# Optimization experiments

Measured on AMD Instinct MI355X. Metric: run time of the kernel, lower is better.

Reference implementation:

```python
import jax, jax.numpy as jnp
import numpy as np

H = 4  # num_heads
EPS = 1e-12


def _mhsa(x, wq, bq, wk, bk, wv, bv, wo, bo):
    # x: [N, A, B, E]; attention over axis B within each (N, A)
    N, A, B, E = x.shape
    d = E // H
    q = (x @ wq + bq).reshape(N, A, B, H, d)
    k = (x @ wk + bk).reshape(N, A, B, H, d)
    v = (x @ wv + bv).reshape(N, A, B, H, d)
    s = jnp.einsum('naqhd,nakhd->nahqk', q, k) / (d ** 0.5)
    a = jax.nn.softmax(s, axis=-1)
    o = jnp.einsum('nahqk,nakhd->naqhd', a, v).reshape(N, A, B, E)
    return o @ wo + bo


def setup_inputs() -> dict:
    key = jax.random.key(0)
    ks = jax.random.split(key, 32)
    N, C, T, V, E, NC = 1024, 3, 30, 14, 64, 7
    g = lambda k, shape, s=0.05: (jax.random.normal(k, shape, dtype=jnp.float32) * s)
    inp = {
        'x_joint': jax.random.normal(ks[0], (N, C, T, V), dtype=jnp.float32),
        'x_vel': jax.random.normal(ks[1], (N, C, T, V), dtype=jnp.float32),
        'je_w': g(ks[2], (C, E)), 'je_b': g(ks[3], (E,)),
        've_w': g(ks[4], (C, E)), 've_b': g(ks[5], (E,)),
        'joint_emb': g(ks[6], (V, E)), 'frame_emb': g(ks[7], (T, E)),
        'proj_w': g(ks[8], (3 * E, E)), 'proj_b': g(ks[9], (E,)),
        'gcn_w1': g(ks[10], (E, E)), 'gcn_b1': g(ks[11], (E,)),
        'gcn_w2': g(ks[12], (E, E)), 'gcn_b2': g(ks[13], (E,)),
        'sa_wq': g(ks[14], (E, E)), 'sa_bq': g(ks[15], (E,)),
        'sa_wk': g(ks[16], (E, E)), 'sa_bk': g(ks[17], (E,)),
        'sa_wv': g(ks[18], (E, E)), 'sa_bv': g(ks[19], (E,)),
        'sa_wo': g(ks[20], (E, E)), 'sa_bo': g(ks[21], (E,)),
        'ta_wq': g(ks[22], (E, E)), 'ta_bq': g(ks[23], (E,)),
        'ta_wk': g(ks[24], (E, E)), 'ta_bk': g(ks[25], (E,)),
        'ta_wv': g(ks[26], (E, E)), 'ta_bv': g(ks[27], (E,)),
        'ta_wo': g(ks[28], (E, E)), 'ta_bo': g(ks[29], (E,)),
        'fc_w': g(ks[30], (E, NC)), 'fc_b': g(ks[31], (NC,)),
    }
    return inp


def reference(x_joint, x_vel, je_w, je_b, ve_w, ve_b, joint_emb, frame_emb,
              proj_w, proj_b, gcn_w1, gcn_b1, gcn_w2, gcn_b2,
              sa_wq, sa_bq, sa_wk, sa_bk, sa_wv, sa_bv, sa_wo, sa_bo,
              ta_wq, ta_bq, ta_wk, ta_bk, ta_wv, ta_bv, ta_wo, ta_bo,
              fc_w, fc_b):
    N, C, T, V = x_joint.shape
    E = je_w.shape[1]
    # 1x1 convs (pointwise over channels) -> [N, T, V, E]
    f = (jnp.einsum('nctv,ce->ntve', x_joint, je_w) + je_b
         + jnp.einsum('nctv,ce->ntve', x_vel, ve_w) + ve_b)
    jE = jnp.broadcast_to(joint_emb[None, None, :, :], (N, T, V, E))
    fE = jnp.broadcast_to(frame_emb[None, :, None, :], (N, T, V, E))
    feat = jnp.concatenate([f, jE, fE], axis=-1) @ proj_w + proj_b  # [N,T,V,E]
    # attention adjacency over joints per frame
    nf = feat / jnp.maximum(jnp.linalg.norm(feat, axis=-1, keepdims=True), EPS)
    adj = jax.nn.softmax(nf @ jnp.swapaxes(nf, -1, -2), axis=-1)  # [N,T,V,V]
    feat = adj @ feat
    feat = jax.nn.relu(feat @ gcn_w1 + gcn_b1) @ gcn_w2 + gcn_b2
    # spatial attention (over V) with residual
    feat = _mhsa(feat, sa_wq, sa_bq, sa_wk, sa_bk, sa_wv, sa_bv, sa_wo, sa_bo) + feat
    # temporal attention (over T) with residual
    ft = jnp.swapaxes(feat, 1, 2)  # [N,V,T,E]
    ft = _mhsa(ft, ta_wq, ta_bq, ta_wk, ta_bk, ta_wv, ta_bv, ta_wo, ta_bo) + ft
    feat = jnp.swapaxes(ft, 1, 2)  # [N,T,V,E]
    pooled = jnp.max(feat, axis=(1, 2))  # adaptive max pool over (T,V)
    return pooled @ fc_w + fc_b
```

## Files before the change

### kernel.cpp

```cpp
#include <hip/hip_runtime.h>
#include <math.h>

#define C_ 3
#define T_ 30
#define V_ 14
#define E_ 64
#define H_ 4
#define D_ 16
#define NC_ 7

#define SW_ 72
#define SV_ 20
#define ARN_ 6272

typedef unsigned short u16;
typedef __attribute__((ext_vector_type(8))) short bf16x8;
typedef __attribute__((ext_vector_type(4))) short bf16x4;
typedef __attribute__((ext_vector_type(4))) float f32x4;
typedef __attribute__((ext_vector_type(16))) float f32x16;

__device__ __forceinline__ float4 f4_load(const float* p) {
    return *reinterpret_cast<const float4*>(p);
}
__device__ __forceinline__ float4 f4_add(float4 a, float4 b) {
    return make_float4(a.x + b.x, a.y + b.y, a.z + b.z, a.w + b.w);
}
__device__ __forceinline__ float4 f4_fma(float a, float4 b, float4 c) {
    c.x = fmaf(a, b.x, c.x); c.y = fmaf(a, b.y, c.y);
    c.z = fmaf(a, b.z, c.z); c.w = fmaf(a, b.w, c.w); return c;
}
__device__ __forceinline__ u16 f2bf(float x) {
    union { __bf16 b; u16 u; } cv;
    cv.b = (__bf16)x;
    return cv.u;
}
__device__ __forceinline__ uint2 pack4bf(float4 f) {
    return make_uint2((unsigned)f2bf(f.x) | ((unsigned)f2bf(f.y) << 16),
                      (unsigned)f2bf(f.z) | ((unsigned)f2bf(f.w) << 16));
}
__device__ __forceinline__ f32x16 f16z() {
    return (f32x16){0.f,0.f,0.f,0.f, 0.f,0.f,0.f,0.f, 0.f,0.f,0.f,0.f, 0.f,0.f,0.f,0.f};
}
__device__ __forceinline__ bf16x8 ld_frag8(const u16* p) {
    bf16x4 lo = *(const bf16x4*)p;
    bf16x4 hi = *(const bf16x4*)(p + 4);
    return __builtin_shufflevector(lo, hi, 0, 1, 2, 3, 4, 5, 6, 7);
}

__global__ void k_setup(const float* __restrict__ je_w, const float* __restrict__ je_b,
                        const float* __restrict__ ve_w, const float* __restrict__ ve_b,
                        const float* __restrict__ joint_emb, const float* __restrict__ frame_emb,
                        const float* __restrict__ proj_w, const float* __restrict__ proj_b,
                        const float* __restrict__ twq, const float* __restrict__ twk,
                        const float* __restrict__ twv, const float* __restrict__ two,
                        const float* __restrict__ sw1, const float* __restrict__ sw2,
                        const float* __restrict__ swq, const float* __restrict__ swk,
                        const float* __restrict__ swv, const float* __restrict__ swo,
                        float* __restrict__ tab) {
    int e = threadIdx.x;
    int b = blockIdx.x;
    if (b >= 1 && b <= 10) {
        int m = b - 1;
        const float* Ws[10] = {twq, twk, twv, two, sw1, sw2, swq, swk, swv, swo};
        const float* W = Ws[m];
        u16* wt = (u16*)(tab + 3200);
        for (int i = 0; i < E_; ++i)
            wt[m * 4096 + e * 64 + i] = f2bf(W[i * E_ + e]);
        return;
    }
    if (b >= 11) {
        float bias = proj_b[e];
        for (int i = 0; i < E_; ++i) bias += (je_b[i] + ve_b[i]) * proj_w[i * E_ + e];
        int t0 = (b - 11) * 10;
        for (int t = t0; t < t0 + 10; ++t) {
            float s = bias;
            for (int i = 0; i < E_; ++i) s += frame_emb[t * E_ + i] * proj_w[(128 + i) * E_ + e];
            tab[1280 + t * E_ + e] = s;
        }
        return;
    }
    for (int c = 0; c < C_; ++c) {
        float aj = 0.f, av = 0.f;
        for (int i = 0; i < E_; ++i) {
            float p0 = proj_w[i * E_ + e];
            aj += je_w[c * E_ + i] * p0;
            av += ve_w[c * E_ + i] * p0;
        }
        tab[c * E_ + e] = aj;
        tab[192 + c * E_ + e] = av;
    }
    for (int v = 0; v < V_; ++v) {
        float s = 0.f;
        for (int i = 0; i < E_; ++i) s += joint_emb[v * E_ + i] * proj_w[(64 + i) * E_ + e];
        tab[384 + v * E_ + e] = s;
    }
}

__global__ __launch_bounds__(128) void k_spatial(
    const float* __restrict__ xj, const float* __restrict__ xv,
    const float* __restrict__ tab, const u16* __restrict__ wt16,
    const float* __restrict__ b1, const float* __restrict__ b2,
    const float* __restrict__ bq, const float* __restrict__ bk,
    const float* __restrict__ bv, const float* __restrict__ bo,
    float* __restrict__ feat1) {
    int ntb0 = blockIdx.x * 2;
    int tid = threadIdx.x;
    int wid = tid >> 6;
    int lane = tid & 63;
    int dcol = lane & 15;
    int kgrp = (lane >> 4) & 3;
    int trow4 = kgrp * 4;
    int e4 = dcol << 2;
    int r4 = kgrp;
    int l32 = lane & 31;
    int half = (lane >> 5) & 1;

    const u16* w1T = wt16 + 4 * 4096;
    const u16* w2T = wt16 + 5 * 4096;
    const u16* wqT = wt16 + 6 * 4096;
    const u16* wkT = wt16 + 7 * 4096;
    const u16* wvT = wt16 + 8 * 4096;
    const u16* woT = wt16 + 9 * 4096;

    __shared__ __align__(16) u16 sm[2 * ARN_];

    int tt[2];
    tt[0] = ntb0 % T_;
    tt[1] = (ntb0 + 1) % T_;
    int nn0 = ntb0 / T_, nn1 = (ntb0 + 1) / T_;

    for (int o = tid; o < 2 * 2 * C_ * V_; o += 128) {
        int tl = o / (2 * C_ * V_);
        int rem = o % (2 * C_ * V_);
        int s = rem / (C_ * V_);
        int r2 = rem % (C_ * V_);
        int c = r2 / V_, v = r2 % V_;
        const float* src = s ? xv : xj;
        int n = tl ? nn1 : nn0;
        float* xs = (float*)(sm + tl * ARN_ + 4992);
        xs[(s * C_ + c) * V_ + v] = src[((size_t)(n * C_ + c) * T_ + tt[tl]) * V_ + v];
    }
    __syncthreads();

    {
        float4 AJ[C_], AV[C_];
#pragma unroll
        for (int c = 0; c < C_; ++c) {
            AJ[c] = f4_load(tab + c * E_ + e4);
            AV[c] = f4_load(tab + 192 + c * E_ + e4);
        }
#pragma unroll
        for (int tl = 0; tl < 2; ++tl) {
            u16* A = sm + tl * ARN_;
            u16* feat16 = A;
            u16* fT16 = A + 1152;
            float* xs = (float*)(A + 4992);
            float4 F = f4_load(tab + 1280 + tt[tl] * E_ + e4);
#pragma unroll
            for (int j = 0; j < 2; ++j) {
                int q = r4 + 4 * (wid * 2 + j);
                if (q < V_) {
                    float4 s = f4_add(F, f4_load(tab + 384 + q * E_ + e4));
#pragma unroll
                    for (int c = 0; c < C_; ++c) {
                        s = f4_fma(xs[(0 * C_ + c) * V_ + q], AJ[c], s);
                        s = f4_fma(xs[(1 * C_ + c) * V_ + q], AV[c], s);
                    }
                    *(uint2*)&feat16[q * SW_ + e4] = pack4bf(s);
                    fT16[(e4 + 0) * SV_ + q] = f2bf(s.x);
                    fT16[(e4 + 1) * SV_ + q] = f2bf(s.y);
                    fT16[(e4 + 2) * SV_ + q] = f2bf(s.z);
                    fT16[(e4 + 3) * SV_ + q] = f2bf(s.w);
                }
            }
        }
        {
            u16* fT16 = sm + wid * ARN_ + 1152;
            fT16[lane * SV_ + 14] = 0;
            fT16[lane * SV_ + 15] = 0;
        }
    }
    __syncthreads();

    {
        u16* A = sm + wid * ARN_;
        u16* feat16 = A;
        float* adjraw = (float*)(A + 2432);
        bf16x8 f0 = *(bf16x8*)&feat16[dcol * SW_ + kgrp * 8];
        bf16x8 f1 = *(bf16x8*)&feat16[dcol * SW_ + 32 + kgrp * 8];
        f32x4 d = (f32x4){0.f, 0.f, 0.f, 0.f};
        d = __builtin_amdgcn_mfma_f32_16x16x32_bf16(f0, f0, d, 0, 0, 0);
        d = __builtin_amdgcn_mfma_f32_16x16x32_bf16(f1, f1, d, 0, 0, 0);
#pragma unroll
        for (int r = 0; r < 4; ++r) {
            int row = trow4 + r;
            if (row < V_) adjraw[row * 18 + dcol] = d[r];
        }
    }
    __syncthreads();

    if (lane < 4 * V_) {
        u16* A = sm + wid * ARN_;
        float* adjraw = (float*)(A + 2432);
        u16* adjs16 = A + 3712;
        int row = lane >> 2, g = lane & 3;
        float iq = 1.0f / fmaxf(sqrtf(adjraw[row * 18 + row]), 1e-12f);
        float c[4];
        float m = -1e30f;
#pragma unroll
        for (int j = 0; j < 4; ++j) {
            int k = g * 4 + j;
            if (k < V_) {
                float ik = 1.0f / fmaxf(sqrtf(adjraw[k * 18 + k]), 1e-12f);
                c[j] = adjraw[row * 18 + k] * iq * ik;
            } else {
                c[j] = -1e30f;
            }
            m = fmaxf(m, c[j]);
        }
        m = fmaxf(m, __shfl_xor(m, 1));
        m = fmaxf(m, __shfl_xor(m, 2));
        float su = 0.f;
#pragma unroll
        for (int j = 0; j < 4; ++j) { c[j] = __expf(c[j] - m); su += c[j]; }
        su += __shfl_xor(su, 1);
        su += __shfl_xor(su, 2);
        float iv = 1.f / su;
#pragma unroll
        for (int j = 0; j < 4; ++j) {
            int k = g * 4 + j;
            if (k < V_) adjs16[row * SV_ + k] = f2bf(c[j] * iv);
        }
        if (g == 3) {
            adjs16[row * SV_ + 14] = 0;
            adjs16[row * SV_ + 15] = 0;
        }
    }
    __syncthreads();

#pragma unroll
    for (int tl = 0; tl < 2; ++tl) {
        u16* A = sm + tl * ARN_;
        u16* adjs16 = A + 3712;
        u16* fT16 = A + 1152;
        u16* g1in = A + 2432;
        bf16x8 aA = ld_frag8(&adjs16[l32 * SV_ + half * 8]);
        int nt = wid;
        bf16x8 bB = ld_frag8(&fT16[(nt * 32 + l32) * SV_ + half * 8]);
        f32x16 g = f16z();
        g = __builtin_amdgcn_mfma_f32_32x32x16_bf16(aA, bB, g, 0, 0, 0);
#pragma unroll
        for (int reg = 0; reg < 16; ++reg) {
            int row = (reg & 3) + 8 * (reg >> 2) + 4 * half;
            if (row < V_) g1in[row * SW_ + nt * 32 + l32] = f2bf(g[reg]);
        }
    }
    __syncthreads();

#pragma unroll
    for (int tl = 0; tl < 2; ++tl) {
        u16* A = sm + tl * ARN_;
        u16* g1in = A + 2432;
        u16* g1out = A;
        bf16x8 a0 = *(bf16x8*)&g1in[dcol * SW_ + kgrp * 8];
        bf16x8 a1 = *(bf16x8*)&g1in[dcol * SW_ + 32 + kgrp * 8];
#pragma unroll
        for (int j = 0; j < 2; ++j) {
            int nt = wid * 2 + j;
            int col = nt * 16 + dcol;
            float bb = b1[col];
            f32x4 cc = (f32x4){bb, bb, bb, bb};
            cc = __builtin_amdgcn_mfma_f32_16x16x32_bf16(a0, *(const bf16x8*)&w1T[col * 64 + kgrp * 8], cc, 0, 0, 0);
            cc = __builtin_amdgcn_mfma_f32_16x16x32_bf16(a1, *(const bf16x8*)&w1T[col * 64 + 32 + kgrp * 8], cc, 0, 0, 0);
#pragma unroll
            for (int r = 0; r < 4; ++r) {
                int row = trow4 + r;
                if (row < V_) g1out[row * SW_ + col] = f2bf(fmaxf(cc[r], 0.f));
            }
        }
    }
    __syncthreads();

    f32x4 fresr[2][2];
#pragma unroll
    for (int tl = 0; tl < 2; ++tl) {
        u16* A = sm + tl * ARN_;
        u16* g1out = A;
        u16* qkvin = A + 1152;
        bf16x8 a0 = *(bf16x8*)&g1out[dcol * SW_ + kgrp * 8];
        bf16x8 a1 = *(bf16x8*)&g1out[dcol * SW_ + 32 + kgrp * 8];
#pragma unroll
        for (int j = 0; j < 2; ++j) {
            int nt = wid * 2 + j;
            int col = nt * 16 + dcol;
            float bb = b2[col];
            f32x4 cc = (f32x4){bb, bb, bb, bb};
            cc = __builtin_amdgcn_mfma_f32_16x16x32_bf16(a0, *(const bf16x8*)&w2T[col * 64 + kgrp * 8], cc, 0, 0, 0);
            cc = __builtin_amdgcn_mfma_f32_16x16x32_bf16(a1, *(const bf16x8*)&w2T[col * 64 + 32 + kgrp * 8], cc, 0, 0, 0);
            fresr[tl][j] = cc;
#pragma unroll
            for (int r = 0; r < 4; ++r) {
                int row = trow4 + r;
                if (row < V_) qkvin[row * SW_ + col] = f2bf(cc[r]);
            }
        }
    }
    __syncthreads();

#pragma unroll
    for (int tl = 0; tl < 2; ++tl) {
        u16* A = sm + tl * ARN_;
        u16* qkvin = A + 1152;
        u16* qs16 = A + 2432;
        u16* ks16 = A + 3712;
        u16* vsT16 = A + 4992;
        bf16x8 a0 = *(bf16x8*)&qkvin[dcol * SW_ + kgrp * 8];
        bf16x8 a1 = *(bf16x8*)&qkvin[dcol * SW_ + 32 + kgrp * 8];
#pragma unroll
        for (int j = 0; j < 2; ++j) {
            int nt = wid * 2 + j;
            int col = nt * 16 + dcol;
            float bqs = bq[col], bks = bk[col], bvs = bv[col];
            f32x4 cq = (f32x4){bqs, bqs, bqs, bqs};
            f32x4 ck = (f32x4){bks, bks, bks, bks};
            f32x4 cv = (f32x4){bvs, bvs, bvs, bvs};
            cq = __builtin_amdgcn_mfma_f32_16x16x32_bf16(a0, *(const bf16x8*)&wqT[col * 64 + kgrp * 8], cq, 0, 0, 0);
            cq = __builtin_amdgcn_mfma_f32_16x16x32_bf16(a1, *(const bf16x8*)&wqT[col * 64 + 32 + kgrp * 8], cq, 0, 0, 0);
            ck = __builtin_amdgcn_mfma_f32_16x16x32_bf16(a0, *(const bf16x8*)&wkT[col * 64 + kgrp * 8], ck, 0, 0, 0);
            ck = __builtin_amdgcn_mfma_f32_16x16x32_bf16(a1, *(const bf16x8*)&wkT[col * 64 + 32 + kgrp * 8], ck, 0, 0, 0);
            cv = __builtin_amdgcn_mfma_f32_16x16x32_bf16(a0, *(const bf16x8*)&wvT[col * 64 + kgrp * 8], cv, 0, 0, 0);
            cv = __builtin_amdgcn_mfma_f32_16x16x32_bf16(a1, *(const bf16x8*)&wvT[col * 64 + 32 + kgrp * 8], cv, 0, 0, 0);
            int pair = wid, hw = j;
            u16* qsb = qs16 + pair * 640;
            u16* ksb = ks16 + pair * 640;
            u16* vtb = vsT16 + pair * 640;
#pragma unroll
            for (int r = 0; r < 4; ++r) {
                int row = trow4 + r;
                qsb[(hw * 16 + row) * SV_ + dcol] = f2bf(cq[r]);
                ksb[(hw * 16 + row) * SV_ + dcol] = f2bf(ck[r]);
                vtb[(hw * 16 + dcol) * SV_ + row] = (row < V_) ? f2bf(cv[r]) : (u16)0;
            }
        }
    }
    __syncthreads();

#pragma unroll
    for (int tl = 0; tl < 2; ++tl) {
        u16* A = sm + tl * ARN_;
        u16* qs16 = A + 2432;
        u16* ks16 = A + 3712;
        float* scb = (float*)A;
        int pair = wid;
        bf16x8 aq = ld_frag8(&qs16[pair * 640 + l32 * SV_ + half * 8]);
        bf16x8 bk8 = ld_frag8(&ks16[pair * 640 + l32 * SV_ + half * 8]);
        f32x16 d = f16z();
        d = __builtin_amdgcn_mfma_f32_32x32x16_bf16(aq, bk8, d, 0, 0, 0);
        int kp = l32 & 15, hp = l32 >> 4;
        if (kp < V_) {
#pragma unroll
            for (int reg = 0; reg < 16; ++reg) {
                int row = (reg & 3) + 8 * (reg >> 2) + 4 * half;
                if ((row >> 4) == hp && (row & 15) < V_)
                    scb[(pair * 2 + hp) * 252 + (row & 15) * 18 + kp] = d[reg];
            }
        }
    }
    __syncthreads();

#pragma unroll
    for (int tl = 0; tl < 2; ++tl) {
        if (lane < 2 * V_) {
            u16* A = sm + tl * ARN_;
            float* scb = (float*)A;
            u16* ps16 = A + 2432;
            int h = wid * 2 + lane / V_, q = lane % V_;
            float p[V_];
            float m = -1e30f;
#pragma unroll
            for (int k = 0; k < V_; ++k) { p[k] = scb[h * 252 + q * 18 + k]; m = fmaxf(m, p[k]); }
            float su = 0.f;
#pragma unroll
            for (int k = 0; k < V_; ++k) { p[k] = __expf((p[k] - m) * 0.25f); su += p[k]; }
            float iv = 1.f / su;
            u16* psb = ps16 + wid * 640;
            int rowp = (h & 1) * 16 + q;
#pragma unroll
            for (int k = 0; k < V_; ++k) psb[rowp * SV_ + k] = f2bf(p[k] * iv);
            psb[rowp * SV_ + 14] = 0;
            psb[rowp * SV_ + 15] = 0;
        }
    }
    __syncthreads();

#pragma unroll
    for (int tl = 0; tl < 2; ++tl) {
        u16* A = sm + tl * ARN_;
        u16* ps16 = A + 2432;
        u16* vsT16 = A + 4992;
        u16* ao16 = A;
        int pair = wid;
        bf16x8 ap = ld_frag8(&ps16[pair * 640 + l32 * SV_ + half * 8]);
        bf16x8 bv8 = ld_frag8(&vsT16[pair * 640 + l32 * SV_ + half * 8]);
        f32x16 d = f16z();
        d = __builtin_amdgcn_mfma_f32_32x32x16_bf16(ap, bv8, d, 0, 0, 0);
        int np = l32 & 15, hp = l32 >> 4;
#pragma unroll
        for (int reg = 0; reg < 16; ++reg) {
            int row = (reg & 3) + 8 * (reg >> 2) + 4 * half;
            if ((row >> 4) == hp && (row & 15) < V_)
                ao16[(row & 15) * SW_ + (pair * 2 + hp) * 16 + np] = f2bf(d[reg]);
        }
    }
    __syncthreads();

#pragma unroll
    for (int tl = 0; tl < 2; ++tl) {
        u16* A = sm + tl * ARN_;
        u16* ao16 = A;
        bf16x8 a0 = *(bf16x8*)&ao16[dcol * SW_ + kgrp * 8];
        bf16x8 a1 = *(bf16x8*)&ao16[dcol * SW_ + 32 + kgrp * 8];
        float* dst = feat1 + (size_t)(ntb0 + tl) * (V_ * E_);
#pragma unroll
        for (int j = 0; j < 2; ++j) {
            int nt = wid * 2 + j;
            int col = nt * 16 + dcol;
            float bos = bo[col];
            f32x4 cc = (f32x4){bos, bos, bos, bos};
            cc = __builtin_amdgcn_mfma_f32_16x16x32_bf16(a0, *(const bf16x8*)&woT[col * 64 + kgrp * 8], cc, 0, 0, 0);
            cc = __builtin_amdgcn_mfma_f32_16x16x32_bf16(a1, *(const bf16x8*)&woT[col * 64 + 32 + kgrp * 8], cc, 0, 0, 0);
#pragma unroll
            for (int r = 0; r < 4; ++r) {
                int row = trow4 + r;
                if (row < V_) dst[row * E_ + col] = cc[r] + fresr[tl][j][r];
            }
        }
    }
}

__global__ __launch_bounds__(64) void k_temporal(
    const float* __restrict__ feat1,
    const u16* __restrict__ wt16,
    const float* __restrict__ bq, const float* __restrict__ bk,
    const float* __restrict__ bv, const float* __restrict__ bo,
    float* __restrict__ tmax) {
    int nv = blockIdx.x;
    int n = nv / V_;
    int v = nv % V_;
    int tid = threadIdx.x;
    int dcol = tid & 15;
    int kgrp = tid >> 4;
    int trow4 = kgrp * 4;
    int l32 = tid & 31;
    int half = tid >> 5;

    const u16* wtq = wt16;
    const u16* wtk = wt16 + 4096;
    const u16* wtv = wt16 + 8192;
    const u16* wto = wt16 + 12288;

    __shared__ __align__(16) u16 smt[6464];
    u16*  ft16 = smt;
    float* scb = (float*)smt;
    u16*  ao16 = smt + 2304;
    u16*  qs16 = smt + 4608;
    u16*  ks16 = smt + 5248;
    u16*  ps16 = smt + 4608;
    u16*  vT16 = smt + 5888;

    const float* fsrc = feat1 + ((size_t)n * T_ * V_ + v) * E_;

    for (int o = tid; o < T_ * 16; o += 64) {
        int t = o >> 4, c4i = (o & 15) << 2;
        float4 f = f4_load(fsrc + (size_t)t * V_ * E_ + c4i);
        *(uint2*)&ft16[t * 72 + c4i] = pack4bf(f);
    }
    __syncthreads();

    bf16x8 af[2][2];
#pragma unroll
    for (int mt = 0; mt < 2; ++mt)
#pragma unroll
        for (int ks = 0; ks < 2; ++ks)
            af[mt][ks] = *(bf16x8*)&ft16[(mt * 16 + dcol) * 72 + ks * 32 + kgrp * 8];

    bool sact = (tid < 2 * T_);
    int sq = sact ? (tid >> 1) : 0;
    int kbase = (tid & 1) * 15;

    for (int h = 0; h < H_; ++h) {
        {
            float bqs = bq[h * D_ + dcol];
            float bks = bk[h * D_ + dcol];
            f32x4 qacc[2], kacc[2];
#pragma unroll
            for (int mt = 0; mt < 2; ++mt) {
                qacc[mt] = (f32x4){bqs, bqs, bqs, bqs};
                kacc[mt] = (f32x4){bks, bks, bks, bks};
            }
#pragma unroll
            for (int ks = 0; ks < 2; ++ks) {
                int boff = (h * D_ + dcol) * 64 + ks * 32 + kgrp * 8;
                bf16x8 b_q = *(const bf16x8*)&wtq[boff];
                bf16x8 b_k = *(const bf16x8*)&wtk[boff];
#pragma unroll
                for (int mt = 0; mt < 2; ++mt) {
                    qacc[mt] = __builtin_amdgcn_mfma_f32_16x16x32_bf16(af[mt][ks], b_q, qacc[mt], 0, 0, 0);
                    kacc[mt] = __builtin_amdgcn_mfma_f32_16x16x32_bf16(af[mt][ks], b_k, kacc[mt], 0, 0, 0);
                }
            }
#pragma unroll
            for (int mt = 0; mt < 2; ++mt)
#pragma unroll
                for (int r = 0; r < 4; ++r) {
                    int t = mt * 16 + trow4 + r;
                    qs16[t * SV_ + dcol] = f2bf(qacc[mt][r]);
                    ks16[t * SV_ + dcol] = f2bf(kacc[mt][r]);
                }
        }
        __syncthreads();

        {
            bf16x8 aq = ld_frag8(&qs16[l32 * SV_ + half * 8]);
            bf16x8 bk8 = ld_frag8(&ks16[l32 * SV_ + half * 8]);
            f32x16 d = f16z();
            d = __builtin_amdgcn_mfma_f32_32x32x16_bf16(aq, bk8, d, 0, 0, 0);
            if (l32 < T_) {
#pragma unroll
                for (int reg = 0; reg < 16; ++reg) {
                    int row = (reg & 3) + 8 * (reg >> 2) + 4 * half;
                    if (row < T_) scb[row * 36 + l32] = d[reg];
                }
            }
        }
        __syncthreads();

        {
            float m = -1e30f;
#pragma unroll
            for (int k = 0; k < 15; ++k) m = fmaxf(m, scb[sq * 36 + kbase + k]);
            m = fmaxf(m, __shfl_xor(m, 1));
            float ex[15];
            float su = 0.f;
#pragma unroll
            for (int k = 0; k < 15; ++k) {
                ex[k] = __expf((scb[sq * 36 + kbase + k] - m) * 0.25f);
                su += ex[k];
            }
            su += __shfl_xor(su, 1);
            float iv = 1.f / su;
            if (sact) {
#pragma unroll
                for (int k = 0; k < 15; ++k) ps16[sq * 36 + kbase + k] = f2bf(ex[k] * iv);
                if (kbase) { ps16[sq * 36 + 30] = 0; ps16[sq * 36 + 31] = 0; }
            }
        }
        {
            float bvs = bv[h * D_ + dcol];
            f32x4 vacc[2];
            vacc[0] = (f32x4){bvs, bvs, bvs, bvs};
            vacc[1] = vacc[0];
#pragma unroll
            for (int ks = 0; ks < 2; ++ks) {
                int boff = (h * D_ + dcol) * 64 + ks * 32 + kgrp * 8;
                bf16x8 b_v = *(const bf16x8*)&wtv[boff];
#pragma unroll
                for (int mt = 0; mt < 2; ++mt)
                    vacc[mt] = __builtin_amdgcn_mfma_f32_16x16x32_bf16(af[mt][ks], b_v, vacc[mt], 0, 0, 0);
            }
#pragma unroll
            for (int mt = 0; mt < 2; ++mt)
#pragma unroll
                for (int r = 0; r < 4; ++r) {
                    int t = mt * 16 + trow4 + r;
                    vT16[dcol * 36 + t] = (t < T_) ? f2bf(vacc[mt][r]) : (u16)0;
                }
        }
        __syncthreads();

        {
            bf16x8 ap0 = ld_frag8(&ps16[l32 * 36 + half * 8]);
            bf16x8 ap1 = ld_frag8(&ps16[l32 * 36 + 16 + half * 8]);
            bf16x8 bv0 = ld_frag8(&vT16[(l32 & 15) * 36 + half * 8]);
            bf16x8 bv1 = ld_frag8(&vT16[(l32 & 15) * 36 + 16 + half * 8]);
            f32x16 d = f16z();
            d = __builtin_amdgcn_mfma_f32_32x32x16_bf16(ap0, bv0, d, 0, 0, 0);
            d = __builtin_amdgcn_mfma_f32_32x32x16_bf16(ap1, bv1, d, 0, 0, 0);
            if (l32 < 16) {
#pragma unroll
                for (int reg = 0; reg < 16; ++reg) {
                    int row = (reg & 3) + 8 * (reg >> 2) + 4 * half;
                    if (row < T_) ao16[row * 72 + h * D_ + l32] = f2bf(d[reg]);
                }
            }
        }
        __syncthreads();
    }

    {
        bf16x8 oa[2][2];
#pragma unroll
        for (int mt = 0; mt < 2; ++mt)
#pragma unroll
            for (int ks = 0; ks < 2; ++ks)
                oa[mt][ks] = *(bf16x8*)&ao16[(mt * 16 + dcol) * 72 + ks * 32 + kgrp * 8];

        float mxc[4];
#pragma unroll
        for (int nt = 0; nt < 4; ++nt) {
            float bos = bo[nt * 16 + dcol];
            f32x4 oacc[2];
            oacc[0] = (f32x4){bos, bos, bos, bos};
            oacc[1] = oacc[0];
#pragma unroll
            for (int ks = 0; ks < 2; ++ks) {
                bf16x8 bb = *(const bf16x8*)&wto[(nt * 16 + dcol) * 64 + ks * 32 + kgrp * 8];
#pragma unroll
                for (int mt = 0; mt < 2; ++mt)
                    oacc[mt] = __builtin_amdgcn_mfma_f32_16x16x32_bf16(oa[mt][ks], bb, oacc[mt], 0, 0, 0);
            }
            float m = -1e30f;
#pragma unroll
            for (int mt = 0; mt < 2; ++mt)
#pragma unroll
                for (int r = 0; r < 4; ++r) {
                    int t = mt * 16 + trow4 + r;
                    if (t < T_) {
                        float rr = oacc[mt][r] +
                                   fsrc[(size_t)t * V_ * E_ + nt * 16 + dcol];
                        m = fmaxf(m, rr);
                    }
                }
            mxc[nt] = m;
        }
#pragma unroll
        for (int nt = 0; nt < 4; ++nt) {
            mxc[nt] = fmaxf(mxc[nt], __shfl_xor(mxc[nt], 16));
            mxc[nt] = fmaxf(mxc[nt], __shfl_xor(mxc[nt], 32));
        }
        if (tid < 16) {
#pragma unroll
            for (int nt = 0; nt < 4; ++nt)
                tmax[(size_t)nv * E_ + nt * 16 + tid] = mxc[nt];
        }
    }
}

__global__ void k_pool_fc(const float* __restrict__ tmax,
                          const float* __restrict__ fc_w, const float* __restrict__ fc_b,
                          float* __restrict__ out) {
    int n = blockIdx.x;
    int tid = threadIdx.x;
    __shared__ float pooled[E_];
    float m = -1e30f;
    for (int v = 0; v < V_; ++v) m = fmaxf(m, tmax[((size_t)n * V_ + v) * E_ + tid]);
    pooled[tid] = m;
    __syncthreads();
    if (tid < NC_) {
        float s = fc_b[tid];
        for (int e = 0; e < E_; ++e) s += pooled[e] * fc_w[e * NC_ + tid];
        out[n * NC_ + tid] = s;
    }
}

extern "C" void kernel_launch(void* const* d_in, const int* in_sizes, int n_in,
                              void* d_out, int out_size, void* d_ws, size_t ws_size,
                              hipStream_t stream) {
    const float* xj        = (const float*)d_in[0];
    const float* xv        = (const float*)d_in[1];
    const float* je_w      = (const float*)d_in[2];
    const float* je_b      = (const float*)d_in[3];
    const float* ve_w      = (const float*)d_in[4];
    const float* ve_b      = (const float*)d_in[5];
    const float* joint_emb = (const float*)d_in[6];
    const float* frame_emb = (const float*)d_in[7];
    const float* proj_w    = (const float*)d_in[8];
    const float* proj_b    = (const float*)d_in[9];
    const float* gcn_w1    = (const float*)d_in[10];
    const float* gcn_b1    = (const float*)d_in[11];
    const float* gcn_w2    = (const float*)d_in[12];
    const float* gcn_b2    = (const float*)d_in[13];
    const float* sa_wq     = (const float*)d_in[14];
    const float* sa_bq     = (const float*)d_in[15];
    const float* sa_wk     = (const float*)d_in[16];
    const float* sa_bk     = (const float*)d_in[17];
    const float* sa_wv     = (const float*)d_in[18];
    const float* sa_bv     = (const float*)d_in[19];
    const float* sa_wo     = (const float*)d_in[20];
    const float* sa_bo     = (const float*)d_in[21];
    const float* ta_wq     = (const float*)d_in[22];
    const float* ta_bq     = (const float*)d_in[23];
    const float* ta_wk     = (const float*)d_in[24];
    const float* ta_bk     = (const float*)d_in[25];
    const float* ta_wv     = (const float*)d_in[26];
    const float* ta_bv     = (const float*)d_in[27];
    const float* ta_wo     = (const float*)d_in[28];
    const float* ta_bo     = (const float*)d_in[29];
    const float* fc_w      = (const float*)d_in[30];
    const float* fc_b      = (const float*)d_in[31];
    float* out = (float*)d_out;

    int N = in_sizes[0] / (C_ * T_ * V_);

    float* ws    = (float*)d_ws;
    float* tab   = ws;
    u16*   wt16  = (u16*)(ws + 3200);
    float* tmax  = ws + 3200 + 20480;
    float* feat1 = tmax + (size_t)N * V_ * E_;

    k_setup<<<14, 64, 0, stream>>>(je_w, je_b, ve_w, ve_b, joint_emb, frame_emb,
                                   proj_w, proj_b,
                                   ta_wq, ta_wk, ta_wv, ta_wo,
                                   gcn_w1, gcn_w2, sa_wq, sa_wk, sa_wv, sa_wo, tab);
    k_spatial<<<N * T_ / 2, 128, 0, stream>>>(xj, xv, tab, wt16,
                                              gcn_b1, gcn_b2,
                                              sa_bq, sa_bk, sa_bv, sa_bo, feat1);
    k_temporal<<<N * V_, 64, 0, stream>>>(feat1, wt16,
                                          ta_bq, ta_bk, ta_bv, ta_bo, tmax);
    k_pool_fc<<<N, 64, 0, stream>>>(tmax, fc_w, fc_b, out);
}
```

Before: 325.0 us.

## Process two (n,v) sequences per temporal-attention block to amortize syncs

The temporal attention kernel now handles two (n,v) sequences per 64-thread block instead of one, with a doubled shared-memory buffer and every phase unrolled over both sequences. This halves the grid size and shares each barrier and the weight-fragment loads across two independent problems, giving the scheduler more independent MFMA and LDS work between syncs. In exchange it raises register use (doubled A fragments) and LDS per block, which may reduce occupancy.

```diff
diff --git a/kernel.cpp b/kernel.cpp
--- a/kernel.cpp
+++ b/kernel.cpp
@@ -12,6 +12,7 @@
 #define SW_ 72
 #define SV_ 20
 #define ARN_ 6272
+#define TRN_ 6464
 
 typedef unsigned short u16;
 typedef __attribute__((ext_vector_type(8))) short bf16x8;
@@ -444,9 +445,7 @@
     const float* __restrict__ bq, const float* __restrict__ bk,
     const float* __restrict__ bv, const float* __restrict__ bo,
     float* __restrict__ tmax) {
-    int nv = blockIdx.x;
-    int n = nv / V_;
-    int v = nv % V_;
+    int nv0 = blockIdx.x * 2;
     int tid = threadIdx.x;
     int dcol = tid & 15;
     int kgrp = tid >> 4;
@@ -459,37 +458,44 @@
     const u16* wtv = wt16 + 8192;
     const u16* wto = wt16 + 12288;
 
-    __shared__ __align__(16) u16 smt[6464];
-    u16*  ft16 = smt;
-    float* scb = (float*)smt;
-    u16*  ao16 = smt + 2304;
-    u16*  qs16 = smt + 4608;
-    u16*  ks16 = smt + 5248;
-    u16*  ps16 = smt + 4608;
-    u16*  vT16 = smt + 5888;
-
-    const float* fsrc = feat1 + ((size_t)n * T_ * V_ + v) * E_;
-
-    for (int o = tid; o < T_ * 16; o += 64) {
-        int t = o >> 4, c4i = (o & 15) << 2;
-        float4 f = f4_load(fsrc + (size_t)t * V_ * E_ + c4i);
-        *(uint2*)&ft16[t * 72 + c4i] = pack4bf(f);
-    }
-    __syncthreads();
-
-    bf16x8 af[2][2];
-#pragma unroll
-    for (int mt = 0; mt < 2; ++mt)
-#pragma unroll
-        for (int ks = 0; ks < 2; ++ks)
-            af[mt][ks] = *(bf16x8*)&ft16[(mt * 16 + dcol) * 72 + ks * 32 + kgrp * 8];
+    __shared__ __align__(16) u16 smt[2 * TRN_];
+
+    const float* fsrc[2];
+    fsrc[0] = feat1 + ((size_t)(nv0 / V_) * T_ * V_ + (nv0 % V_)) * E_;
+    fsrc[1] = feat1 + ((size_t)((nv0 + 1) / V_) * T_ * V_ + ((nv0 + 1) % V_)) * E_;
+
+#pragma unroll
+    for (int tl = 0; tl < 2; ++tl) {
+        u16* ft16 = smt + tl * TRN_;
+        for (int o = tid; o < T_ * 16; o += 64) {
+            int t = o >> 4, c4i = (o & 15) << 2;
+            float4 f = f4_load(fsrc[tl] + (size_t)t * V_ * E_ + c4i);
+            *(uint2*)&ft16[t * 72 + c4i] = pack4bf(f);
+        }
+    }
+    __syncthreads();
+
+    bf16x8 af[2][2][2];
+#pragma unroll
+    for (int tl = 0; tl < 2; ++tl) {
+        u16* ft16 = smt + tl * TRN_;
+#pragma unroll
+        for (int mt = 0; mt < 2; ++mt)
+#pragma unroll
+            for (int ks = 0; ks < 2; ++ks)
+                af[tl][mt][ks] = *(bf16x8*)&ft16[(mt * 16 + dcol) * 72 + ks * 32 + kgrp * 8];
+    }
 
     bool sact = (tid < 2 * T_);
     int sq = sact ? (tid >> 1) : 0;
     int kbase = (tid & 1) * 15;
 
     for (int h = 0; h < H_; ++h) {
-        {
+#pragma unroll
+        for (int tl = 0; tl < 2; ++tl) {
+            u16* A = smt + tl * TRN_;
+            u16* qs16 = A + 4608;
+            u16* ks16 = A + 5248;
             float bqs = bq[h * D_ + dcol];
             float bks = bk[h * D_ + dcol];
             f32x4 qacc[2], kacc[2];
@@ -505,8 +511,8 @@
                 bf16x8 b_k = *(const bf16x8*)&wtk[boff];
 #pragma unroll
                 for (int mt = 0; mt < 2; ++mt) {
-                    qacc[mt] = __builtin_amdgcn_mfma_f32_16x16x32_bf16(af[mt][ks], b_q, qacc[mt], 0, 0, 0);
-                    kacc[mt] = __builtin_amdgcn_mfma_f32_16x16x32_bf16(af[mt][ks], b_k, kacc[mt], 0, 0, 0);
+                    qacc[mt] = __builtin_amdgcn_mfma_f32_16x16x32_bf16(af[tl][mt][ks], b_q, qacc[mt], 0, 0, 0);
+                    kacc[mt] = __builtin_amdgcn_mfma_f32_16x16x32_bf16(af[tl][mt][ks], b_k, kacc[mt], 0, 0, 0);
                 }
             }
 #pragma unroll
@@ -520,7 +526,12 @@
         }
         __syncthreads();
 
-        {
+#pragma unroll
+        for (int tl = 0; tl < 2; ++tl) {
+            u16* A = smt + tl * TRN_;
+            u16* qs16 = A + 4608;
+            u16* ks16 = A + 5248;
+            float* scb = (float*)A;
             bf16x8 aq = ld_frag8(&qs16[l32 * SV_ + half * 8]);
             bf16x8 bk8 = ld_frag8(&ks16[l32 * SV_ + half * 8]);
             f32x16 d = f16z();
@@ -535,50 +546,62 @@
         }
         __syncthreads();
 
-        {
-            float m = -1e30f;
-#pragma unroll
-            for (int k = 0; k < 15; ++k) m = fmaxf(m, scb[sq * 36 + kbase + k]);
-            m = fmaxf(m, __shfl_xor(m, 1));
-            float ex[15];
-            float su = 0.f;
-#pragma unroll
-            for (int k = 0; k < 15; ++k) {
-                ex[k] = __expf((scb[sq * 36 + kbase + k] - m) * 0.25f);
-                su += ex[k];
-            }
-            su += __shfl_xor(su, 1);
-            float iv = 1.f / su;
-            if (sact) {
-#pragma unroll
-                for (int k = 0; k < 15; ++k) ps16[sq * 36 + kbase + k] = f2bf(ex[k] * iv);
-                if (kbase) { ps16[sq * 36 + 30] = 0; ps16[sq * 36 + 31] = 0; }
-            }
-        }
-        {
-            float bvs = bv[h * D_ + dcol];
-            f32x4 vacc[2];
-            vacc[0] = (f32x4){bvs, bvs, bvs, bvs};
-            vacc[1] = vacc[0];
-#pragma unroll
-            for (int ks = 0; ks < 2; ++ks) {
-                int boff = (h * D_ + dcol) * 64 + ks * 32 + kgrp * 8;
-                bf16x8 b_v = *(const bf16x8*)&wtv[boff];
+#pragma unroll
+        for (int tl = 0; tl < 2; ++tl) {
+            u16* A = smt + tl * TRN_;
+            float* scb = (float*)A;
+            u16* ps16 = A + 4608;
+            u16* vT16 = A + 5888;
+            {
+                float m = -1e30f;
+#pragma unroll
+                for (int k = 0; k < 15; ++k) m = fmaxf(m, scb[sq * 36 + kbase + k]);
+                m = fmaxf(m, __shfl_xor(m, 1));
+                float ex[15];
+                float su = 0.f;
+#pragma unroll
+                for (int k = 0; k < 15; ++k) {
+                    ex[k] = __expf((scb[sq * 36 + kbase + k] - m) * 0.25f);
+                    su += ex[k];
+                }
+                su += __shfl_xor(su, 1);
+                float iv = 1.f / su;
+                if (sact) {
+#pragma unroll
+                    for (int k = 0; k < 15; ++k) ps16[sq * 36 + kbase + k] = f2bf(ex[k] * iv);
+                    if (kbase) { ps16[sq * 36 + 30] = 0; ps16[sq * 36 + 31] = 0; }
+                }
+            }
+            {
+                float bvs = bv[h * D_ + dcol];
+                f32x4 vacc[2];
+                vacc[0] = (f32x4){bvs, bvs, bvs, bvs};
+                vacc[1] = vacc[0];
+#pragma unroll
+                for (int ks = 0; ks < 2; ++ks) {
+                    int boff = (h * D_ + dcol) * 64 + ks * 32 + kgrp * 8;
+                    bf16x8 b_v = *(const bf16x8*)&wtv[boff];
+#pragma unroll
+                    for (int mt = 0; mt < 2; ++mt)
+                        vacc[mt] = __builtin_amdgcn_mfma_f32_16x16x32_bf16(af[tl][mt][ks], b_v, vacc[mt], 0, 0, 0);
+                }
 #pragma unroll
                 for (int mt = 0; mt < 2; ++mt)
-                    vacc[mt] = __builtin_amdgcn_mfma_f32_16x16x32_bf16(af[mt][ks], b_v, vacc[mt], 0, 0, 0);
-            }
-#pragma unroll
-            for (int mt = 0; mt < 2; ++mt)
-#pragma unroll
-                for (int r = 0; r < 4; ++r) {
-                    int t = mt * 16 + trow4 + r;
-                    vT16[dcol * 36 + t] = (t < T_) ? f2bf(vacc[mt][r]) : (u16)0;
-                }
+#pragma unroll
+                    for (int r = 0; r < 4; ++r) {
+                        int t = mt * 16 + trow4 + r;
+                        vT16[dcol * 36 + t] = (t < T_) ? f2bf(vacc[mt][r]) : (u16)0;
+                    }
+            }
         }
         __syncthreads();
 
-        {
+#pragma unroll
+        for (int tl = 0; tl < 2; ++tl) {
+            u16* A = smt + tl * TRN_;
+            u16* ps16 = A + 4608;
+            u16* vT16 = A + 5888;
+            u16* ao16 = A + 2304;
             bf16x8 ap0 = ld_frag8(&ps16[l32 * 36 + half * 8]);
             bf16x8 ap1 = ld_frag8(&ps16[l32 * 36 + 16 + half * 8]);
             bf16x8 bv0 = ld_frag8(&vT16[(l32 & 15) * 36 + half * 8]);
@@ -597,7 +620,9 @@
         __syncthreads();
     }
 
-    {
+#pragma unroll
+    for (int tl = 0; tl < 2; ++tl) {
+        u16* ao16 = smt + tl * TRN_ + 2304;
         bf16x8 oa[2][2];
 #pragma unroll
         for (int mt = 0; mt < 2; ++mt)
@@ -627,7 +652,7 @@
                     int t = mt * 16 + trow4 + r;
                     if (t < T_) {
                         float rr = oacc[mt][r] +
-                                   fsrc[(size_t)t * V_ * E_ + nt * 16 + dcol];
+                                   fsrc[tl][(size_t)t * V_ * E_ + nt * 16 + dcol];
                         m = fmaxf(m, rr);
                     }
                 }
@@ -641,7 +666,7 @@
         if (tid < 16) {
 #pragma unroll
             for (int nt = 0; nt < 4; ++nt)
-                tmax[(size_t)nv * E_ + nt * 16 + tid] = mxc[nt];
+                tmax[(size_t)(nv0 + tl) * E_ + nt * 16 + tid] = mxc[nt];
         }
     }
 }
@@ -715,7 +740,7 @@
     k_spatial<<<N * T_ / 2, 128, 0, stream>>>(xj, xv, tab, wt16,
                                               gcn_b1, gcn_b2,
                                               sa_bq, sa_bk, sa_bv, sa_bo, feat1);
-    k_temporal<<<N * V_, 64, 0, stream>>>(feat1, wt16,
-                                          ta_bq, ta_bk, ta_bv, ta_bo, tmax);
+    k_temporal<<<N * V_ / 2, 64, 0, stream>>>(feat1, wt16,
+                                              ta_bq, ta_bk, ta_bv, ta_bo, tmax);
     k_pool_fc<<<N, 64, 0, stream>>>(tmax, fc_w, fc_b, out);
 }
```

New measurement: 371.6 us. 1.14x slower.
